# Kernel optimization log

Hardware: AMD Instinct MI355X
Metric: run time of the kernel (lower is better)

Reference implementation:

```python
import jax, jax.numpy as jnp
import numpy as np
from jax.scipy.stats import norm

N_TOK = 4096
D_MODEL = 1024
D_FF = 2048
N_EXP = 8
K = 2
NOISE_EPS = 0.01          # noise_epsilon in noisy_top_k_gating
LOSS_COEF = 0.1
ZERO_FILL = float(np.finfo(float).eps)  # combined[combined == 0] = eps


def setup_inputs() -> dict:
    key = jax.random.key(0)
    ks = jax.random.split(key, 8)
    s = 0.02
    return {
        "x": jax.random.normal(ks[0], (N_TOK, D_MODEL), jnp.float32),
        "noise": jax.random.normal(ks[1], (N_TOK, N_EXP), jnp.float32),  # torch.randn_like(clean_logits)
        "w_gate": jax.random.normal(ks[2], (D_MODEL, N_EXP), jnp.float32) * s,
        "w_noise": jax.random.normal(ks[3], (D_MODEL, N_EXP), jnp.float32) * s,
        "w1": jax.random.normal(ks[4], (N_EXP, D_MODEL, D_FF), jnp.float32) * s,
        "b1": jnp.zeros((N_EXP, D_FF), jnp.float32),
        "w2": jax.random.normal(ks[5], (N_EXP, D_FF, D_MODEL), jnp.float32) * s,
        "b2": jnp.zeros((N_EXP, D_MODEL), jnp.float32),
    }


def _cv_squared(v):
    # torch .var() is unbiased (ddof=1)
    return jnp.var(v, ddof=1) / (jnp.mean(v) ** 2 + 1e-10)


def reference(x, noise, w_gate, w_noise, w1, b1, w2, b2):
    B = x.shape[0]
    # --- noisy top-k gating (train=True) ---
    clean_logits = x @ w_gate                                   # [B, E]
    noise_stddev = jax.nn.softplus(x @ w_noise) + NOISE_EPS     # [B, E]
    noisy_logits = clean_logits + noise * noise_stddev
    m = min(K + 1, N_EXP)
    top_vals, top_idx = jax.lax.top_k(noisy_logits, m)          # [B, k+1]
    top_k_gates = jax.nn.softmax(top_vals[:, :K], axis=1)       # [B, k]
    gates = jnp.zeros((B, N_EXP), x.dtype).at[
        jnp.arange(B)[:, None], top_idx[:, :K]
    ].set(top_k_gates)                                          # [B, E] sparse-in-values

    # --- load via _prob_in_top_k ---
    thr_in = top_vals[:, K][:, None]       # (k+1)-th noisy value
    thr_out = top_vals[:, K - 1][:, None]  # k-th noisy value
    is_in = noisy_logits > thr_in
    prob_if_in = norm.cdf((clean_logits - thr_in) / noise_stddev)
    prob_if_out = norm.cdf((clean_logits - thr_out) / noise_stddev)
    load = jnp.where(is_in, prob_if_in, prob_if_out).sum(0)     # [E]

    importance = gates.sum(0)
    loss = (_cv_squared(importance) + _cv_squared(load)) * LOSS_COEF

    # --- expert FFNs + gate-weighted combine ---
    # Dense-over-experts evaluation; gates are zero for non-selected experts,
    # so this is mathematically identical to dispatch/combine.
    h = jax.nn.relu(jnp.einsum('td,edf->tef', x, w1) + b1)      # [T, E, d_ff]
    expert_out = jnp.einsum('tef,efd->ted', h, w2) + b2         # [T, E, d_model]
    y = jnp.einsum('ted,te->td', expert_out, gates)             # [T, d_model]
    y = jnp.where(y == 0, ZERO_FILL, y)                         # combined[combined==0] = eps
    return y, loss
```

## Files before the change

### kernel.cpp

```cpp
#include <hip/hip_runtime.h>
#include <hip/hip_bf16.h>

#define N_TOK 4096
#define D_MODEL 1024
#define D_FF 2048
#define N_EXP 8

typedef __attribute__((ext_vector_type(8))) short short8;
typedef __attribute__((ext_vector_type(4))) float f32x4;

#define OFF_COUNTS 0
#define OFF_BASE   64
#define OFF_SEL    128
#define OFF_G0     16512
#define OFF_TOK    32896
#define OFF_SLOT   163968
#define OFF_GATE   295040
#define OFF_LOADV  426112
#define OFF_XB     1048576
#define OFF_W1T    9437184
#define OFF_W2T    42991616
#define OFF_H      76546048
#define OFF_SOUT   110100480

__device__ __forceinline__ unsigned short f2bf(float f) {
  union { float f; unsigned u; } a; a.f = f;
  return (unsigned short)((a.u + 0x7FFFu + ((a.u >> 16) & 1u)) >> 16);
}

__device__ __forceinline__ void async16(const void* g, void* l) {
  __builtin_amdgcn_global_load_lds(
      (const __attribute__((address_space(1))) unsigned int*)g,
      (__attribute__((address_space(3))) unsigned int*)l, 16, 0, 0);
}

__global__ __launch_bounds__(256) void convert_x_kernel(
    const float* __restrict__ x, unsigned short* __restrict__ xb, int* counts) {
  if (blockIdx.x == 0 && threadIdx.x < N_EXP) counts[threadIdx.x] = 0;
  const int i = blockIdx.x * 256 + threadIdx.x;
  float4 v = ((const float4*)x)[i];
  ushort4 o;
  o.x = f2bf(v.x); o.y = f2bf(v.y); o.z = f2bf(v.z); o.w = f2bf(v.w);
  ((ushort4*)xb)[i] = o;
}

__global__ __launch_bounds__(256) void transpose_bf16_kernel(
    const float* __restrict__ in, unsigned short* __restrict__ out, int K, int N) {
  __shared__ float tile[32][33];
  const int e = blockIdx.z;
  const int kb = blockIdx.y * 32, nb = blockIdx.x * 32;
  const int c = threadIdx.x & 31, r0 = threadIdx.x >> 5;
  const float* ine = in + (size_t)e * K * N;
  unsigned short* oute = out + (size_t)e * K * N;
#pragma unroll
  for (int i = 0; i < 4; ++i)
    tile[r0 + i * 8][c] = ine[(size_t)(kb + r0 + i * 8) * N + nb + c];
  __syncthreads();
#pragma unroll
  for (int i = 0; i < 4; ++i)
    oute[(size_t)(nb + r0 + i * 8) * K + kb + c] = f2bf(tile[c][r0 + i * 8]);
}

__global__ __launch_bounds__(256) void gating_kernel(
    const float* __restrict__ x, const float* __restrict__ noise,
    const float* __restrict__ wg, const float* __restrict__ wn,
    int* __restrict__ sel, float* __restrict__ g0out,
    float* __restrict__ loadvec) {
  const int wave = threadIdx.x >> 6, lane = threadIdx.x & 63;
  const int t = blockIdx.x * 4 + wave;
  float ag[8], an[8];
#pragma unroll
  for (int e = 0; e < 8; ++e) { ag[e] = 0.f; an[e] = 0.f; }
  const float* xrow = x + (size_t)t * D_MODEL;
  for (int d = lane; d < D_MODEL; d += 64) {
    const float xv = xrow[d];
    const float4 wa = ((const float4*)(wg + (size_t)d * 8))[0];
    const float4 wb = ((const float4*)(wg + (size_t)d * 8))[1];
    const float4 na = ((const float4*)(wn + (size_t)d * 8))[0];
    const float4 nb = ((const float4*)(wn + (size_t)d * 8))[1];
    ag[0] += xv * wa.x; ag[1] += xv * wa.y; ag[2] += xv * wa.z; ag[3] += xv * wa.w;
    ag[4] += xv * wb.x; ag[5] += xv * wb.y; ag[6] += xv * wb.z; ag[7] += xv * wb.w;
    an[0] += xv * na.x; an[1] += xv * na.y; an[2] += xv * na.z; an[3] += xv * na.w;
    an[4] += xv * nb.x; an[5] += xv * nb.y; an[6] += xv * nb.z; an[7] += xv * nb.w;
  }
#pragma unroll
  for (int e = 0; e < 8; ++e) {
#pragma unroll
    for (int off = 32; off > 0; off >>= 1) {
      ag[e] += __shfl_xor(ag[e], off, 64);
      an[e] += __shfl_xor(an[e], off, 64);
    }
  }
  float clean[8], sd[8], nz[8];
#pragma unroll
  for (int e = 0; e < 8; ++e) {
    clean[e] = ag[e];
    float s = an[e];
    s = (s > 20.f) ? s : log1pf(expf(s));
    sd[e] = s + 0.01f;
    nz[e] = clean[e] + noise[t * 8 + e] * sd[e];
  }
  float v0 = -1e30f, v1 = -1e30f, v2 = -1e30f; int i0 = 0, i1 = 0;
#pragma unroll
  for (int e = 0; e < 8; ++e) {
    const float v = nz[e];
    if (v > v0)      { v2 = v1; v1 = v0; i1 = i0; v0 = v; i0 = e; }
    else if (v > v1) { v2 = v1; v1 = v; i1 = e; }
    else if (v > v2) { v2 = v; }
  }
  const float ex = expf(v1 - v0);
  const float g0 = 1.f / (1.f + ex);
  if (lane == 0) { sel[t] = i0 | (i1 << 8); g0out[t] = g0; }
  if (lane < 8) {
    const int e = lane;
    const bool is_in = nz[e] > v2;
    const float thr = is_in ? v2 : v1;
    const float z = (clean[e] - thr) / sd[e];
    loadvec[t * 8 + e] = 0.5f * erfcf(-z * 0.70710678118654752f);
  }
}

__global__ __launch_bounds__(256) void build_lists_kernel(
    const int* __restrict__ sel, const float* __restrict__ g0a,
    int* __restrict__ counts, int* __restrict__ tok_list,
    int* __restrict__ slot_list, float* __restrict__ gate_list) {
  __shared__ int hist[8], bbase[8];
  if (threadIdx.x < 8) hist[threadIdx.x] = 0;
  __syncthreads();
  const int t = blockIdx.x * 256 + threadIdx.x;
  const int s = sel[t];
  const int e0 = s & 255, e1 = (s >> 8) & 255;
  atomicAdd(&hist[e0], 1);
  atomicAdd(&hist[e1], 1);
  __syncthreads();
  if (threadIdx.x < 8) {
    bbase[threadIdx.x] = atomicAdd(&counts[threadIdx.x], hist[threadIdx.x]);
    hist[threadIdx.x] = 0;
  }
  __syncthreads();
  const float g = g0a[t];
  const int p0 = atomicAdd(&hist[e0], 1);
  const int idx0 = e0 * N_TOK + bbase[e0] + p0;
  tok_list[idx0] = t; slot_list[idx0] = 0; gate_list[idx0] = g;
  const int p1 = atomicAdd(&hist[e1], 1);
  const int idx1 = e1 * N_TOK + bbase[e1] + p1;
  tok_list[idx1] = t; slot_list[idx1] = 1; gate_list[idx1] = 1.f - g;
}

__global__ __launch_bounds__(256) void loss_scan_kernel(
    const int* __restrict__ counts, int* __restrict__ base,
    const int* __restrict__ sel, const float* __restrict__ g0a,
    const float* __restrict__ loadvec, float* __restrict__ loss_out) {
  float limp[8], lld[8];
#pragma unroll
  for (int e = 0; e < 8; ++e) { limp[e] = 0.f; lld[e] = 0.f; }
  for (int t = threadIdx.x; t < N_TOK; t += 256) {
    const int s = sel[t];
    const float g = g0a[t];
    const int e0 = s & 255, e1 = (s >> 8) & 255;
#pragma unroll
    for (int e = 0; e < 8; ++e)
      limp[e] += (e0 == e ? g : 0.f) + (e1 == e ? (1.f - g) : 0.f);
#pragma unroll
    for (int e = 0; e < 8; ++e) lld[e] += loadvec[t * 8 + e];
  }
#pragma unroll
  for (int e = 0; e < 8; ++e) {
#pragma unroll
    for (int off = 32; off > 0; off >>= 1) {
      limp[e] += __shfl_xor(limp[e], off, 64);
      lld[e]  += __shfl_xor(lld[e],  off, 64);
    }
  }
  __shared__ float red[4][16];
  const int wave = threadIdx.x >> 6, lane = threadIdx.x & 63;
  if (lane == 0) {
#pragma unroll
    for (int e = 0; e < 8; ++e) { red[wave][e] = limp[e]; red[wave][8 + e] = lld[e]; }
  }
  __syncthreads();
  if (threadIdx.x == 0) {
    double imp[8], ld[8];
    for (int e = 0; e < 8; ++e) {
      imp[e] = (double)red[0][e] + red[1][e] + red[2][e] + red[3][e];
      ld[e]  = (double)red[0][8 + e] + red[1][8 + e] + red[2][8 + e] + red[3][8 + e];
    }
    double mi = 0, ml = 0;
    for (int e = 0; e < 8; ++e) { mi += imp[e]; ml += ld[e]; }
    mi /= 8.0; ml /= 8.0;
    double vi = 0, vl = 0;
    for (int e = 0; e < 8; ++e) { vi += (imp[e] - mi) * (imp[e] - mi); vl += (ld[e] - ml) * (ld[e] - ml); }
    vi /= 7.0; vl /= 7.0;
    const double loss = 0.1 * (vi / (mi * mi + 1e-10) + vl / (ml * ml + 1e-10));
    loss_out[0] = (float)loss;
    int b = 0;
    for (int e = 0; e < 8; ++e) { base[e] = b; b += counts[e]; }
  }
}

__global__ __launch_bounds__(256) void gemm1_kernel(
    const unsigned short* __restrict__ xb, const unsigned short* __restrict__ w1t,
    const float* __restrict__ b1,
    const int* __restrict__ counts, const int* __restrict__ base,
    const int* __restrict__ tok_list, unsigned short* __restrict__ h) {
  const int e = blockIdx.x, nt = blockIdx.y, mt = blockIdx.z;
  const int cnt = counts[e];
  const int m0 = mt * 128;
  if (m0 >= cnt) return;
  const int n0 = nt * 128;
  const int bs = base[e];

  __shared__ __align__(16) unsigned short As[128 * 64];
  __shared__ __align__(16) unsigned short Bs[128 * 64];

  const int tid = threadIdx.x;
  const int wave = tid >> 6, lane = tid & 63;
  const int lrow = lane >> 3;
  const int scg  = (lane & 7) ^ lrow;

  const unsigned short* ap[4];
  const unsigned short* bp[4];
  unsigned short* adst[4];
  unsigned short* bdst[4];
#pragma unroll
  for (int c = 0; c < 4; ++c) {
    const int rr = wave * 32 + c * 8;
    const int arow = min(m0 + rr + lrow, cnt - 1);
    const int tok = tok_list[e * N_TOK + arow];
    ap[c] = xb + (size_t)tok * D_MODEL + scg * 8;
    bp[c] = w1t + (size_t)e * D_MODEL * D_FF + (size_t)(n0 + rr + lrow) * D_MODEL + scg * 8;
    adst[c] = As + rr * 64;
    bdst[c] = Bs + rr * 64;
  }

  const int wm = wave & 1, wn = wave >> 1;
  const int q = lane >> 4, r = lane & 15;
  const int r7 = r & 7;

  f32x4 acc[4][4];
#pragma unroll
  for (int a = 0; a < 4; ++a)
#pragma unroll
    for (int b = 0; b < 4; ++b) acc[a][b] = (f32x4){0.f, 0.f, 0.f, 0.f};

  for (int k0 = 0; k0 < D_MODEL; k0 += 64) {
#pragma unroll
    for (int c = 0; c < 4; ++c) {
      async16(ap[c], adst[c]);
      async16(bp[c], bdst[c]);
      ap[c] += 64; bp[c] += 64;
    }
    __syncthreads();
#pragma unroll
    for (int kk = 0; kk < 64; kk += 32) {
      const int gsw = (((kk >> 3) + q) ^ r7) * 8;
      short8 af[4], bfg[4];
#pragma unroll
      for (int t = 0; t < 4; ++t)
        af[t] = *(const short8*)(As + (wm * 64 + t * 16 + r) * 64 + gsw);
#pragma unroll
      for (int t = 0; t < 4; ++t)
        bfg[t] = *(const short8*)(Bs + (wn * 64 + t * 16 + r) * 64 + gsw);
#pragma unroll
      for (int tm = 0; tm < 4; ++tm)
#pragma unroll
        for (int tn = 0; tn < 4; ++tn)
          acc[tm][tn] = __builtin_amdgcn_mfma_f32_16x16x32_bf16(af[tm], bfg[tn], acc[tm][tn], 0, 0, 0);
    }
    __syncthreads();
  }

  float bv[4];
#pragma unroll
  for (int tn = 0; tn < 4; ++tn) bv[tn] = b1[e * D_FF + n0 + wn * 64 + tn * 16 + r];
#pragma unroll
  for (int tm = 0; tm < 4; ++tm) {
#pragma unroll
    for (int v = 0; v < 4; ++v) {
      const int i = wm * 64 + tm * 16 + q * 4 + v;
      if (m0 + i < cnt) {
        unsigned short* hrow = h + (size_t)(bs + m0 + i) * D_FF + n0 + wn * 64 + r;
#pragma unroll
        for (int tn = 0; tn < 4; ++tn)
          hrow[tn * 16] = f2bf(fmaxf(acc[tm][tn][v] + bv[tn], 0.f));
      }
    }
  }
}

__global__ __launch_bounds__(256) void gemm2_kernel(
    const unsigned short* __restrict__ h, const unsigned short* __restrict__ w2t,
    const float* __restrict__ b2,
    const int* __restrict__ counts, const int* __restrict__ base,
    const int* __restrict__ tok_list, const int* __restrict__ slot_list,
    const float* __restrict__ gate_list, float* __restrict__ sout) {
  const int e = blockIdx.x, nt = blockIdx.y, mt = blockIdx.z;
  const int cnt = counts[e];
  const int m0 = mt * 128;
  if (m0 >= cnt) return;
  const int n0 = nt * 128;
  const int bs = base[e];

  __shared__ __align__(16) unsigned short As[128 * 64];
  __shared__ __align__(16) unsigned short Bs[128 * 64];

  const int tid = threadIdx.x;
  const int wave = tid >> 6, lane = tid & 63;
  const int lrow = lane >> 3;
  const int scg  = (lane & 7) ^ lrow;

  const unsigned short* ap[4];
  const unsigned short* bp[4];
  unsigned short* adst[4];
  unsigned short* bdst[4];
#pragma unroll
  for (int c = 0; c < 4; ++c) {
    const int rr = wave * 32 + c * 8;
    const int arow = min(m0 + rr + lrow, cnt - 1);
    ap[c] = h + (size_t)(bs + arow) * D_FF + scg * 8;
    bp[c] = w2t + (size_t)e * D_MODEL * D_FF + (size_t)(n0 + rr + lrow) * D_FF + scg * 8;
    adst[c] = As + rr * 64;
    bdst[c] = Bs + rr * 64;
  }

  const int wm = wave & 1, wn = wave >> 1;
  const int q = lane >> 4, r = lane & 15;
  const int r7 = r & 7;

  f32x4 acc[4][4];
#pragma unroll
  for (int a = 0; a < 4; ++a)
#pragma unroll
    for (int b = 0; b < 4; ++b) acc[a][b] = (f32x4){0.f, 0.f, 0.f, 0.f};

  for (int k0 = 0; k0 < D_FF; k0 += 64) {
#pragma unroll
    for (int c = 0; c < 4; ++c) {
      async16(ap[c], adst[c]);
      async16(bp[c], bdst[c]);
      ap[c] += 64; bp[c] += 64;
    }
    __syncthreads();
#pragma unroll
    for (int kk = 0; kk < 64; kk += 32) {
      const int gsw = (((kk >> 3) + q) ^ r7) * 8;
      short8 af[4], bfg[4];
#pragma unroll
      for (int t = 0; t < 4; ++t)
        af[t] = *(const short8*)(As + (wm * 64 + t * 16 + r) * 64 + gsw);
#pragma unroll
      for (int t = 0; t < 4; ++t)
        bfg[t] = *(const short8*)(Bs + (wn * 64 + t * 16 + r) * 64 + gsw);
#pragma unroll
      for (int tm = 0; tm < 4; ++tm)
#pragma unroll
        for (int tn = 0; tn < 4; ++tn)
          acc[tm][tn] = __builtin_amdgcn_mfma_f32_16x16x32_bf16(af[tm], bfg[tn], acc[tm][tn], 0, 0, 0);
    }
    __syncthreads();
  }

  float bv[4];
#pragma unroll
  for (int tn = 0; tn < 4; ++tn) bv[tn] = b2[e * D_MODEL + n0 + wn * 64 + tn * 16 + r];
#pragma unroll
  for (int tm = 0; tm < 4; ++tm) {
#pragma unroll
    for (int v = 0; v < 4; ++v) {
      const int i = wm * 64 + tm * 16 + q * 4 + v;
      const int mrow = m0 + i;
      if (mrow < cnt) {
        const int idx = e * N_TOK + mrow;
        const int tok = tok_list[idx];
        const int sl = slot_list[idx];
        const float g = gate_list[idx];
        float* orow = sout + ((size_t)sl * N_TOK + tok) * D_MODEL + n0 + wn * 64 + r;
#pragma unroll
        for (int tn = 0; tn < 4; ++tn)
          orow[tn * 16] = (acc[tm][tn][v] + bv[tn]) * g;
      }
    }
  }
}

__global__ __launch_bounds__(256) void combine_kernel(
    const float* __restrict__ sout, float* __restrict__ y) {
  const int i = blockIdx.x * 256 + threadIdx.x;
  const float4 a = ((const float4*)sout)[i];
  const float4 b = ((const float4*)(sout + (size_t)N_TOK * D_MODEL))[i];
  float4 o;
  o.x = a.x + b.x; o.y = a.y + b.y; o.z = a.z + b.z; o.w = a.w + b.w;
  const float eps = 2.2204460492503131e-16f;
  if (o.x == 0.f) o.x = eps;
  if (o.y == 0.f) o.y = eps;
  if (o.z == 0.f) o.z = eps;
  if (o.w == 0.f) o.w = eps;
  ((float4*)y)[i] = o;
}

extern "C" void kernel_launch(void* const* d_in, const int* in_sizes, int n_in,
                              void* d_out, int out_size, void* d_ws, size_t ws_size,
                              hipStream_t stream) {
  const float* x     = (const float*)d_in[0];
  const float* noise = (const float*)d_in[1];
  const float* wg    = (const float*)d_in[2];
  const float* wn    = (const float*)d_in[3];
  const float* w1    = (const float*)d_in[4];
  const float* b1    = (const float*)d_in[5];
  const float* w2    = (const float*)d_in[6];
  const float* b2    = (const float*)d_in[7];
  float* out = (float*)d_out;

  char* ws = (char*)d_ws;
  int*   counts    = (int*)(ws + OFF_COUNTS);
  int*   base      = (int*)(ws + OFF_BASE);
  int*   sel       = (int*)(ws + OFF_SEL);
  float* g0a       = (float*)(ws + OFF_G0);
  int*   tok_list  = (int*)(ws + OFF_TOK);
  int*   slot_list = (int*)(ws + OFF_SLOT);
  float* gate_list = (float*)(ws + OFF_GATE);
  float* loadvec   = (float*)(ws + OFF_LOADV);
  unsigned short* xb  = (unsigned short*)(ws + OFF_XB);
  unsigned short* w1t = (unsigned short*)(ws + OFF_W1T);
  unsigned short* w2t = (unsigned short*)(ws + OFF_W2T);
  unsigned short* h   = (unsigned short*)(ws + OFF_H);
  float* sout = (float*)(ws + OFF_SOUT);

  convert_x_kernel<<<4096, 256, 0, stream>>>(x, xb, counts);
  transpose_bf16_kernel<<<dim3(D_FF / 32, D_MODEL / 32, N_EXP), 256, 0, stream>>>(w1, w1t, D_MODEL, D_FF);
  transpose_bf16_kernel<<<dim3(D_MODEL / 32, D_FF / 32, N_EXP), 256, 0, stream>>>(w2, w2t, D_FF, D_MODEL);
  gating_kernel<<<N_TOK / 4, 256, 0, stream>>>(x, noise, wg, wn, sel, g0a, loadvec);
  build_lists_kernel<<<N_TOK / 256, 256, 0, stream>>>(sel, g0a, counts, tok_list, slot_list, gate_list);
  loss_scan_kernel<<<1, 256, 0, stream>>>(counts, base, sel, g0a, loadvec,
                                          out + (size_t)N_TOK * D_MODEL);
  gemm1_kernel<<<dim3(N_EXP, D_FF / 128, N_TOK / 128), 256, 0, stream>>>(
      xb, w1t, b1, counts, base, tok_list, h);
  gemm2_kernel<<<dim3(N_EXP, D_MODEL / 128, N_TOK / 128), 256, 0, stream>>>(
      h, w2t, b2, counts, base, tok_list, slot_list, gate_list, sout);
  combine_kernel<<<(N_TOK * D_MODEL / 4) / 256, 256, 0, stream>>>(sout, out);
}
```

Before: 358.6 us.

## Fuse x conversion into gating, widen transpose tiles, split-K gemm2

Conversion of x to bf16 moves into the gating kernel, which drops one launch and one full read of x. The weight transpose kernel now uses 64x64 tiles with float4 loads and 16-byte bf16 stores. gemm2 is split into two K-halves, which doubles the number of blocks for better CU occupancy; the halves write to two separate partial buffers, the second reusing the w1t region, and the combine kernel sums four inputs instead of two. The cost is extra partial-output traffic in gemm2 and combine.

```diff
diff --git a/kernel.cpp b/kernel.cpp
--- a/kernel.cpp
+++ b/kernel.cpp
@@ -34,38 +34,46 @@
       (__attribute__((address_space(3))) unsigned int*)l, 16, 0, 0);
 }
 
-__global__ __launch_bounds__(256) void convert_x_kernel(
-    const float* __restrict__ x, unsigned short* __restrict__ xb, int* counts) {
-  if (blockIdx.x == 0 && threadIdx.x < N_EXP) counts[threadIdx.x] = 0;
-  const int i = blockIdx.x * 256 + threadIdx.x;
-  float4 v = ((const float4*)x)[i];
-  ushort4 o;
-  o.x = f2bf(v.x); o.y = f2bf(v.y); o.z = f2bf(v.z); o.w = f2bf(v.w);
-  ((ushort4*)xb)[i] = o;
-}
-
 __global__ __launch_bounds__(256) void transpose_bf16_kernel(
     const float* __restrict__ in, unsigned short* __restrict__ out, int K, int N) {
-  __shared__ float tile[32][33];
+  __shared__ float tile[64][65];
   const int e = blockIdx.z;
-  const int kb = blockIdx.y * 32, nb = blockIdx.x * 32;
-  const int c = threadIdx.x & 31, r0 = threadIdx.x >> 5;
+  const int kb = blockIdx.y * 64, nb = blockIdx.x * 64;
+  const int tid = threadIdx.x;
   const float* ine = in + (size_t)e * K * N;
   unsigned short* oute = out + (size_t)e * K * N;
-#pragma unroll
-  for (int i = 0; i < 4; ++i)
-    tile[r0 + i * 8][c] = ine[(size_t)(kb + r0 + i * 8) * N + nb + c];
+  {
+    const int c4 = tid & 15;
+    const int rr = tid >> 4;
+#pragma unroll
+    for (int i = 0; i < 4; ++i) {
+      const int row = i * 16 + rr;
+      const float4 v = *(const float4*)(ine + (size_t)(kb + row) * N + nb + c4 * 4);
+      tile[row][c4 * 4 + 0] = v.x;
+      tile[row][c4 * 4 + 1] = v.y;
+      tile[row][c4 * 4 + 2] = v.z;
+      tile[row][c4 * 4 + 3] = v.w;
+    }
+  }
   __syncthreads();
-#pragma unroll
-  for (int i = 0; i < 4; ++i)
-    oute[(size_t)(nb + r0 + i * 8) * K + kb + c] = f2bf(tile[c][r0 + i * 8]);
+  {
+    const int n = tid >> 2, seg = tid & 3;
+    unsigned short v[16];
+#pragma unroll
+    for (int j = 0; j < 16; ++j) v[j] = f2bf(tile[seg * 16 + j][n]);
+    uint4* dst = (uint4*)(oute + (size_t)(nb + n) * K + kb + seg * 16);
+    dst[0] = *(uint4*)&v[0];
+    dst[1] = *(uint4*)&v[8];
+  }
 }
 
 __global__ __launch_bounds__(256) void gating_kernel(
     const float* __restrict__ x, const float* __restrict__ noise,
     const float* __restrict__ wg, const float* __restrict__ wn,
     int* __restrict__ sel, float* __restrict__ g0out,
-    float* __restrict__ loadvec) {
+    float* __restrict__ loadvec, unsigned short* __restrict__ xb,
+    int* __restrict__ counts) {
+  if (blockIdx.x == 0 && threadIdx.x < N_EXP) counts[threadIdx.x] = 0;
   const int wave = threadIdx.x >> 6, lane = threadIdx.x & 63;
   const int t = blockIdx.x * 4 + wave;
   float ag[8], an[8];
@@ -82,6 +90,17 @@
     ag[4] += xv * wb.x; ag[5] += xv * wb.y; ag[6] += xv * wb.z; ag[7] += xv * wb.w;
     an[0] += xv * na.x; an[1] += xv * na.y; an[2] += xv * na.z; an[3] += xv * na.w;
     an[4] += xv * nb.x; an[5] += xv * nb.y; an[6] += xv * nb.z; an[7] += xv * nb.w;
+  }
+  {
+    const float4* xv4 = (const float4*)xrow;
+    ushort4* xb4 = (ushort4*)(xb + (size_t)t * D_MODEL);
+#pragma unroll
+    for (int i = 0; i < 4; ++i) {
+      const float4 v = xv4[lane + i * 64];
+      ushort4 o;
+      o.x = f2bf(v.x); o.y = f2bf(v.y); o.z = f2bf(v.z); o.w = f2bf(v.w);
+      xb4[lane + i * 64] = o;
+    }
   }
 #pragma unroll
   for (int e = 0; e < 8; ++e) {
@@ -293,13 +312,16 @@
     const float* __restrict__ b2,
     const int* __restrict__ counts, const int* __restrict__ base,
     const int* __restrict__ tok_list, const int* __restrict__ slot_list,
-    const float* __restrict__ gate_list, float* __restrict__ sout) {
-  const int e = blockIdx.x, nt = blockIdx.y, mt = blockIdx.z;
+    const float* __restrict__ gate_list,
+    float* __restrict__ sout0, float* __restrict__ sout1) {
+  const int e = blockIdx.x, nt = blockIdx.y;
+  const int mt = blockIdx.z >> 1, kh = blockIdx.z & 1;
   const int cnt = counts[e];
   const int m0 = mt * 128;
   if (m0 >= cnt) return;
   const int n0 = nt * 128;
   const int bs = base[e];
+  const int kbase = kh * (D_FF / 2);
 
   __shared__ __align__(16) unsigned short As[128 * 64];
   __shared__ __align__(16) unsigned short Bs[128 * 64];
@@ -317,8 +339,8 @@
   for (int c = 0; c < 4; ++c) {
     const int rr = wave * 32 + c * 8;
     const int arow = min(m0 + rr + lrow, cnt - 1);
-    ap[c] = h + (size_t)(bs + arow) * D_FF + scg * 8;
-    bp[c] = w2t + (size_t)e * D_MODEL * D_FF + (size_t)(n0 + rr + lrow) * D_FF + scg * 8;
+    ap[c] = h + (size_t)(bs + arow) * D_FF + kbase + scg * 8;
+    bp[c] = w2t + (size_t)e * D_MODEL * D_FF + (size_t)(n0 + rr + lrow) * D_FF + kbase + scg * 8;
     adst[c] = As + rr * 64;
     bdst[c] = Bs + rr * 64;
   }
@@ -333,7 +355,7 @@
 #pragma unroll
     for (int b = 0; b < 4; ++b) acc[a][b] = (f32x4){0.f, 0.f, 0.f, 0.f};
 
-  for (int k0 = 0; k0 < D_FF; k0 += 64) {
+  for (int k0 = 0; k0 < D_FF / 2; k0 += 64) {
 #pragma unroll
     for (int c = 0; c < 4; ++c) {
       async16(ap[c], adst[c]);
@@ -362,7 +384,9 @@
 
   float bv[4];
 #pragma unroll
-  for (int tn = 0; tn < 4; ++tn) bv[tn] = b2[e * D_MODEL + n0 + wn * 64 + tn * 16 + r];
+  for (int tn = 0; tn < 4; ++tn)
+    bv[tn] = (kh == 0) ? b2[e * D_MODEL + n0 + wn * 64 + tn * 16 + r] : 0.f;
+  float* const souts = (kh == 0) ? sout0 : sout1;
 #pragma unroll
   for (int tm = 0; tm < 4; ++tm) {
 #pragma unroll
@@ -374,7 +398,7 @@
         const int tok = tok_list[idx];
         const int sl = slot_list[idx];
         const float g = gate_list[idx];
-        float* orow = sout + ((size_t)sl * N_TOK + tok) * D_MODEL + n0 + wn * 64 + r;
+        float* orow = souts + ((size_t)sl * N_TOK + tok) * D_MODEL + n0 + wn * 64 + r;
 #pragma unroll
         for (int tn = 0; tn < 4; ++tn)
           orow[tn * 16] = (acc[tm][tn][v] + bv[tn]) * g;
@@ -384,12 +408,18 @@
 }
 
 __global__ __launch_bounds__(256) void combine_kernel(
-    const float* __restrict__ sout, float* __restrict__ y) {
+    const float* __restrict__ sout0, const float* __restrict__ sout1,
+    float* __restrict__ y) {
   const int i = blockIdx.x * 256 + threadIdx.x;
-  const float4 a = ((const float4*)sout)[i];
-  const float4 b = ((const float4*)(sout + (size_t)N_TOK * D_MODEL))[i];
+  const float4 a = ((const float4*)sout0)[i];
+  const float4 b = ((const float4*)(sout0 + (size_t)N_TOK * D_MODEL))[i];
+  const float4 c = ((const float4*)sout1)[i];
+  const float4 d = ((const float4*)(sout1 + (size_t)N_TOK * D_MODEL))[i];
   float4 o;
-  o.x = a.x + b.x; o.y = a.y + b.y; o.z = a.z + b.z; o.w = a.w + b.w;
+  o.x = (a.x + c.x) + (b.x + d.x);
+  o.y = (a.y + c.y) + (b.y + d.y);
+  o.z = (a.z + c.z) + (b.z + d.z);
+  o.w = (a.w + c.w) + (b.w + d.w);
   const float eps = 2.2204460492503131e-16f;
   if (o.x == 0.f) o.x = eps;
   if (o.y == 0.f) o.y = eps;
@@ -424,18 +454,18 @@
   unsigned short* w1t = (unsigned short*)(ws + OFF_W1T);
   unsigned short* w2t = (unsigned short*)(ws + OFF_W2T);
   unsigned short* h   = (unsigned short*)(ws + OFF_H);
-  float* sout = (float*)(ws + OFF_SOUT);
-
-  convert_x_kernel<<<4096, 256, 0, stream>>>(x, xb, counts);
-  transpose_bf16_kernel<<<dim3(D_FF / 32, D_MODEL / 32, N_EXP), 256, 0, stream>>>(w1, w1t, D_MODEL, D_FF);
-  transpose_bf16_kernel<<<dim3(D_MODEL / 32, D_FF / 32, N_EXP), 256, 0, stream>>>(w2, w2t, D_FF, D_MODEL);
-  gating_kernel<<<N_TOK / 4, 256, 0, stream>>>(x, noise, wg, wn, sel, g0a, loadvec);
+  float* sout0 = (float*)(ws + OFF_SOUT);
+  float* sout1 = (float*)(ws + OFF_W1T);
+
+  gating_kernel<<<N_TOK / 4, 256, 0, stream>>>(x, noise, wg, wn, sel, g0a, loadvec, xb, counts);
+  transpose_bf16_kernel<<<dim3(D_FF / 64, D_MODEL / 64, N_EXP), 256, 0, stream>>>(w1, w1t, D_MODEL, D_FF);
+  transpose_bf16_kernel<<<dim3(D_MODEL / 64, D_FF / 64, N_EXP), 256, 0, stream>>>(w2, w2t, D_FF, D_MODEL);
   build_lists_kernel<<<N_TOK / 256, 256, 0, stream>>>(sel, g0a, counts, tok_list, slot_list, gate_list);
   loss_scan_kernel<<<1, 256, 0, stream>>>(counts, base, sel, g0a, loadvec,
                                           out + (size_t)N_TOK * D_MODEL);
   gemm1_kernel<<<dim3(N_EXP, D_FF / 128, N_TOK / 128), 256, 0, stream>>>(
       xb, w1t, b1, counts, base, tok_list, h);
-  gemm2_kernel<<<dim3(N_EXP, D_MODEL / 128, N_TOK / 128), 256, 0, stream>>>(
-      h, w2t, b2, counts, base, tok_list, slot_list, gate_list, sout);
-  combine_kernel<<<(N_TOK * D_MODEL / 4) / 256, 256, 0, stream>>>(sout, out);
-}
+  gemm2_kernel<<<dim3(N_EXP, D_MODEL / 128, (N_TOK / 128) * 2), 256, 0, stream>>>(
+      h, w2t, b2, counts, base, tok_list, slot_list, gate_list, sout0, sout1);
+  combine_kernel<<<(N_TOK * D_MODEL / 4) / 256, 256, 0, stream>>>(sout0, sout1, out);
+}
```

Result: faster. 350.4 us (-2.3%).
